# Optimization experiments

Hardware: AMD Instinct MI355X
Metric: run time of the kernel (lower is better)

## Reference

```python
import jax, jax.numpy as jnp
import numpy as np

N_NODES = 100000
N_EDGES = 3200000
ALPHA = 0.1
ITERATIONS = 10


def setup_inputs() -> dict:
    key = jax.random.key(0)
    ks = jax.random.split(key, 7)
    features = jax.random.normal(ks[0], (N_NODES, 512), dtype=jnp.float32)
    W1 = jax.random.normal(ks[1], (512, 64), dtype=jnp.float32) * 0.05
    b1 = jax.random.normal(ks[2], (64,), dtype=jnp.float32) * 0.05
    W2 = jax.random.normal(ks[3], (64, 64), dtype=jnp.float32) * 0.05
    b2 = jax.random.normal(ks[4], (64,), dtype=jnp.float32) * 0.05
    edge_weights = jax.random.uniform(ks[5], (N_EDGES,), dtype=jnp.float32)
    edge_index = jax.random.randint(ks[6], (2, N_EDGES), 0, N_NODES, dtype=jnp.int64)
    return {"features": features, "W1": W1, "b1": b1, "W2": W2, "b2": b2,
            "edge_weights": edge_weights, "edge_index": edge_index}


def reference(features, W1, b1, W2, b2, edge_weights, edge_index):
    # dense MLP head (dropout disabled / eval mode)
    h = jax.nn.relu(features @ W1 + b1)          # [N, hidden]
    z = h @ W2 + b2                              # [N, labels]

    row, col = edge_index[0], edge_index[1]

    def step(p, _):
        # SpMM: out[row] += w * p[col]
        gathered = edge_weights[:, None] * p[col]                 # [E, labels]
        new = jax.ops.segment_sum(gathered, row, num_segments=N_NODES)
        p = (1.0 - ALPHA) * new + ALPHA * z
        return p, None

    p, _ = jax.lax.scan(step, z, None, length=ITERATIONS)
    return p
```

## Files before the change

kernel.cpp:

```cpp
#include <hip/hip_runtime.h>
#include <hip/hip_fp16.h>
#include <cmath>

#define N_NODES 100000
#define N_EDGES 3200000
#define ALPHA   0.1f
#define ITERS   10
#define NBUK    1024
#define RPB     98
#define CHUNK   16384
#define NCH     196

typedef __attribute__((ext_vector_type(8))) short short8;
typedef __attribute__((ext_vector_type(4))) float f32x4;

__device__ __forceinline__ short f2bf(float x) {
    union { float f; unsigned u; } v; v.f = x;
    unsigned r = v.u + 0x7fffu + ((v.u >> 16) & 1u);
    return (short)(r >> 16);
}

__global__ void prep_w(const float* __restrict__ W1, const float* __restrict__ W2,
                       short* __restrict__ W1t, short* __restrict__ W2t)
{
    int t = blockIdx.x * 256 + threadIdx.x;
    if (t < 512 * 64) { int k = t >> 6, c = t & 63; W1t[c * 512 + k] = f2bf(W1[t]); }
    if (t < 64 * 64)  { int k = t >> 6, c = t & 63; W2t[c * 64 + k]  = f2bf(W2[t]); }
}

__global__ __launch_bounds__(256) void mlp_mfma(
    const float* __restrict__ F, const short* __restrict__ W1t,
    const short* __restrict__ W2t, const float* __restrict__ b1,
    const float* __restrict__ b2, __half* __restrict__ q0)
{
    __shared__ short Ft[64 * 128];
    __shared__ short Ht[64 * 64];

    const int t  = threadIdx.x;
    const int l  = t & 63;
    const int wv = t >> 6;
    const int wr = wv * 16;
    const long base = (long)blockIdx.x * 64;

    const int sr = t >> 4;
    const int sk = (t & 15) * 8;

    float4 f0a, f0b, f1a, f1b, f2a, f2b, f3a, f3b;

#define LOAD_TILE(kt) do {                                                   \
    long g0 = base + sr;      if (g0 > N_NODES - 1) g0 = N_NODES - 1;        \
    long g1 = base + sr + 16; if (g1 > N_NODES - 1) g1 = N_NODES - 1;        \
    long g2 = base + sr + 32; if (g2 > N_NODES - 1) g2 = N_NODES - 1;        \
    long g3 = base + sr + 48; if (g3 > N_NODES - 1) g3 = N_NODES - 1;        \
    f0a = *(const float4*)(F + g0 * 512 + (kt) * 128 + sk);                  \
    f0b = *(const float4*)(F + g0 * 512 + (kt) * 128 + sk + 4);              \
    f1a = *(const float4*)(F + g1 * 512 + (kt) * 128 + sk);                  \
    f1b = *(const float4*)(F + g1 * 512 + (kt) * 128 + sk + 4);              \
    f2a = *(const float4*)(F + g2 * 512 + (kt) * 128 + sk);                  \
    f2b = *(const float4*)(F + g2 * 512 + (kt) * 128 + sk + 4);              \
    f3a = *(const float4*)(F + g3 * 512 + (kt) * 128 + sk);                  \
    f3b = *(const float4*)(F + g3 * 512 + (kt) * 128 + sk + 4);              \
} while (0)

#define STORE_ROW(row, fa, fb) do {                                          \
    int r_ = (row);                                                          \
    short8 s_ = { f2bf((fa).x), f2bf((fa).y), f2bf((fa).z), f2bf((fa).w),    \
                  f2bf((fb).x), f2bf((fb).y), f2bf((fb).z), f2bf((fb).w) };  \
    *(short8*)&Ft[(r_ * 128 + sk) ^ ((r_ & 7) << 3)] = s_;                   \
} while (0)

    LOAD_TILE(0);

    f32x4 acc[4] = {};
    for (int kt = 0; kt < 4; ++kt) {
        STORE_ROW(sr,      f0a, f0b);
        STORE_ROW(sr + 16, f1a, f1b);
        STORE_ROW(sr + 32, f2a, f2b);
        STORE_ROW(sr + 48, f3a, f3b);
        __syncthreads();
        if (kt < 3) LOAD_TILE(kt + 1);
#pragma unroll
        for (int kc = 0; kc < 4; ++kc) {
            int kb = kc * 32 + (l >> 4) * 8;
            int ar = wr + (l & 15);
            short8 a = *(const short8*)&Ft[(ar * 128 + kb) ^ ((ar & 7) << 3)];
#pragma unroll
            for (int n = 0; n < 4; ++n) {
                int bc = n * 16 + (l & 15);
                short8 b = *(const short8*)(W1t + bc * 512 + kt * 128 + kb);
                acc[n] = __builtin_amdgcn_mfma_f32_16x16x32_bf16(a, b, acc[n], 0, 0, 0);
            }
        }
        __syncthreads();
    }

#pragma unroll
    for (int n = 0; n < 4; ++n) {
        int col = n * 16 + (l & 15);
        float bv = b1[col];
#pragma unroll
        for (int i = 0; i < 4; ++i) {
            int row = wr + (l >> 4) * 4 + i;
            float hv = fmaxf(acc[n][i] + bv, 0.0f);
            Ht[(row * 64 + col) ^ ((row & 7) << 3)] = f2bf(hv);
        }
    }
    f32x4 acc2[4] = {};
#pragma unroll
    for (int kc = 0; kc < 2; ++kc) {
        int kb = kc * 32 + (l >> 4) * 8;
        int ar = wr + (l & 15);
        short8 a = *(const short8*)&Ht[(ar * 64 + kb) ^ ((ar & 7) << 3)];
#pragma unroll
        for (int n = 0; n < 4; ++n) {
            int bc = n * 16 + (l & 15);
            short8 b = *(const short8*)(W2t + bc * 64 + kb);
            acc2[n] = __builtin_amdgcn_mfma_f32_16x16x32_bf16(a, b, acc2[n], 0, 0, 0);
        }
    }
#pragma unroll
    for (int n = 0; n < 4; ++n) {
        int col = n * 16 + (l & 15);
        float bv = b2[col];
#pragma unroll
        for (int i = 0; i < 4; ++i) {
            long row = base + wr + (l >> 4) * 4 + i;
            if (row < N_NODES)
                q0[row * 64 + col] = __float2half(acc2[n][i] + bv);
        }
    }
#undef LOAD_TILE
#undef STORE_ROW
}

__global__ __launch_bounds__(256) void bhist(const int* __restrict__ rows, int* __restrict__ gh)
{
    __shared__ int cnt[NBUK];
    for (int i = threadIdx.x; i < NBUK; i += 256) cnt[i] = 0;
    __syncthreads();
    int base = blockIdx.x * CHUNK;
    int end  = base + CHUNK; if (end > N_EDGES) end = N_EDGES;
    for (int i = base + threadIdx.x; i < end; i += 256)
        atomicAdd(&cnt[rows[i] / RPB], 1);
    __syncthreads();
    for (int i = threadIdx.x; i < NBUK; i += 256)
        gh[i * NCH + blockIdx.x] = cnt[i];
}

__global__ __launch_bounds__(512) void bscan(int* __restrict__ gh, int* __restrict__ btot)
{
    __shared__ int s[512];
    int k = blockIdx.x;
    int t = threadIdx.x;
    int v = (t < NCH) ? gh[k * NCH + t] : 0;
    s[t] = v;
    __syncthreads();
    for (int off = 1; off < 512; off <<= 1) {
        int x = (t >= off) ? s[t - off] : 0;
        __syncthreads();
        s[t] += x;
        __syncthreads();
    }
    if (t < NCH) gh[k * NCH + t] = s[t] - v;
    if (t == NCH - 1) btot[k] = s[t];
}

__global__ __launch_bounds__(1024) void scan_btot(const int* __restrict__ btot, int* __restrict__ bbase)
{
    __shared__ int s[1024];
    int t = threadIdx.x;
    int v = btot[t];
    s[t] = v;
    __syncthreads();
    for (int off = 1; off < 1024; off <<= 1) {
        int x = (t >= off) ? s[t - off] : 0;
        __syncthreads();
        s[t] += x;
        __syncthreads();
    }
    bbase[t] = s[t] - v;
}

__global__ __launch_bounds__(256) void bpart(const int* __restrict__ rows, const int* __restrict__ cols,
                                             const float* __restrict__ w, const int* __restrict__ gh,
                                             const int* __restrict__ bbase, uint2* __restrict__ stg)
{
    __shared__ int cur[NBUK];
    int blk = blockIdx.x;
    for (int i = threadIdx.x; i < NBUK; i += 256)
        cur[i] = bbase[i] + gh[i * NCH + blk];
    __syncthreads();
    int base = blk * CHUNK;
    int end  = base + CHUNK; if (end > N_EDGES) end = N_EDGES;
    for (int i = base + threadIdx.x; i < end; i += 256) {
        int r = rows[i];
        int b = r / RPB;
        int pos = atomicAdd(&cur[b], 1);
        float ws = w[i] * ((1.0f - ALPHA) / 16.0f);
        unsigned meta = (unsigned)cols[i] | ((unsigned)(r - b * RPB) << 17);
        stg[pos] = make_uint2(meta, __float_as_uint(ws));
    }
}

__global__ __launch_bounds__(256) void bucket_sort2(const int* __restrict__ bbase,
                                                    const uint2* __restrict__ stg,
                                                    unsigned long long* __restrict__ cw,
                                                    int* __restrict__ rowp)
{
    __shared__ int ldeg[RPB];
    __shared__ int lcur[RPB];
    __shared__ int sc[128];
    const int b = blockIdx.x;
    const int rowlo = b * RPB;
    if (rowlo >= N_NODES) return;
    int rowhi = rowlo + RPB; if (rowhi > N_NODES) rowhi = N_NODES;
    const int nrows = rowhi - rowlo;
    const int t = threadIdx.x;
    const int base = bbase[b];
    const int cnt = ((b + 1 < NBUK) ? bbase[b + 1] : N_EDGES) - base;

    if (t < RPB) ldeg[t] = 0;
    __syncthreads();
    for (int j = t; j < cnt; j += 256)
        atomicAdd(&ldeg[stg[base + j].x >> 17], 1);
    __syncthreads();
    int v = 0;
    if (t < 128) { v = (t < nrows) ? ldeg[t] : 0; sc[t] = v; }
    __syncthreads();
    for (int off = 1; off < 128; off <<= 1) {
        int x = (t < 128 && t >= off) ? sc[t - off] : 0;
        __syncthreads();
        if (t < 128) sc[t] += x;
        __syncthreads();
    }
    if (t < nrows) {
        int rp = base + sc[t] - v;
        rowp[rowlo + t] = rp;
        lcur[t] = rp;
    }
    if (t == 0 && rowhi == N_NODES) rowp[N_NODES] = base + cnt;
    __syncthreads();
    for (int j = t; j < cnt; j += 256) {
        uint2 rec = stg[base + j];
        int roff = rec.x >> 17;
        unsigned col = rec.x & 0x1FFFFu;
        int pos = atomicAdd(&lcur[roff], 1);
        cw[pos] = (unsigned long long)col | ((unsigned long long)rec.y << 32);
    }
}

template <int LAST>
__global__ __launch_bounds__(256) void spmm_kernel(
    const int* __restrict__ rowp, const unsigned long long* __restrict__ cw,
    const __half* __restrict__ qin, const __half* __restrict__ zh,
    float beta, float outscale,
    __half* __restrict__ qout, float* __restrict__ out)
{
    const int wid = blockIdx.x * 4 + (threadIdx.x >> 6);
    if (wid >= N_NODES) return;
    const int lane = threadIdx.x & 63;
    const int sub  = lane >> 3;
    const int l8   = lane & 7;

    const int start = rowp[wid];
    const int end   = rowp[wid + 1];

    uint4 zv = *(const uint4*)(zh + (long)wid * 64 + l8 * 8);

    float a0 = 0, a1 = 0, a2 = 0, a3 = 0, a4 = 0, a5 = 0, a6 = 0, a7 = 0;

#define ACC_EDGE(pc, v)                                                       \
    do {                                                                      \
        float ww_ = __uint_as_float((unsigned)((pc) >> 32));                  \
        float2 p_;                                                            \
        p_ = __half22float2(*(__half2*)&(v).x); a0 += ww_ * p_.x; a1 += ww_ * p_.y; \
        p_ = __half22float2(*(__half2*)&(v).y); a2 += ww_ * p_.x; a3 += ww_ * p_.y; \
        p_ = __half22float2(*(__half2*)&(v).z); a4 += ww_ * p_.x; a5 += ww_ * p_.y; \
        p_ = __half22float2(*(__half2*)&(v).w); a6 += ww_ * p_.x; a7 += ww_ * p_.y; \
    } while (0)

    int e = start + sub;
    for (; e + 24 < end; e += 32) {
        unsigned long long pc0 = cw[e];
        unsigned long long pc1 = cw[e + 8];
        unsigned long long pc2 = cw[e + 16];
        unsigned long long pc3 = cw[e + 24];
        uint4 v0 = *(const uint4*)(qin + (long)(unsigned)pc0 * 64 + l8 * 8);
        uint4 v1 = *(const uint4*)(qin + (long)(unsigned)pc1 * 64 + l8 * 8);
        uint4 v2 = *(const uint4*)(qin + (long)(unsigned)pc2 * 64 + l8 * 8);
        uint4 v3 = *(const uint4*)(qin + (long)(unsigned)pc3 * 64 + l8 * 8);
        ACC_EDGE(pc0, v0);
        ACC_EDGE(pc1, v1);
        ACC_EDGE(pc2, v2);
        ACC_EDGE(pc3, v3);
    }
    for (; e < end; e += 8) {
        unsigned long long pc = cw[e];
        uint4 v = *(const uint4*)(qin + (long)(unsigned)pc * 64 + l8 * 8);
        ACC_EDGE(pc, v);
    }
#undef ACC_EDGE

    a0 += __shfl_xor(a0, 8);  a1 += __shfl_xor(a1, 8);
    a2 += __shfl_xor(a2, 8);  a3 += __shfl_xor(a3, 8);
    a4 += __shfl_xor(a4, 8);  a5 += __shfl_xor(a5, 8);
    a6 += __shfl_xor(a6, 8);  a7 += __shfl_xor(a7, 8);
    a0 += __shfl_xor(a0, 16); a1 += __shfl_xor(a1, 16);
    a2 += __shfl_xor(a2, 16); a3 += __shfl_xor(a3, 16);
    a4 += __shfl_xor(a4, 16); a5 += __shfl_xor(a5, 16);
    a6 += __shfl_xor(a6, 16); a7 += __shfl_xor(a7, 16);
    a0 += __shfl_xor(a0, 32); a1 += __shfl_xor(a1, 32);
    a2 += __shfl_xor(a2, 32); a3 += __shfl_xor(a3, 32);
    a4 += __shfl_xor(a4, 32); a5 += __shfl_xor(a5, 32);
    a6 += __shfl_xor(a6, 32); a7 += __shfl_xor(a7, 32);

    if (lane < 8) {
        float2 z0 = __half22float2(*(__half2*)&zv.x);
        float2 z1 = __half22float2(*(__half2*)&zv.y);
        float2 z2 = __half22float2(*(__half2*)&zv.z);
        float2 z3 = __half22float2(*(__half2*)&zv.w);
        float o0 = a0 + beta * z0.x, o1 = a1 + beta * z0.y;
        float o2 = a2 + beta * z1.x, o3 = a3 + beta * z1.y;
        float o4 = a4 + beta * z2.x, o5 = a5 + beta * z2.y;
        float o6 = a6 + beta * z3.x, o7 = a7 + beta * z3.y;
        if (LAST) {
            float4 ra = { outscale * o0, outscale * o1, outscale * o2, outscale * o3 };
            float4 rb = { outscale * o4, outscale * o5, outscale * o6, outscale * o7 };
            *(float4*)(out + (long)wid * 64 + lane * 8)     = ra;
            *(float4*)(out + (long)wid * 64 + lane * 8 + 4) = rb;
        } else {
            __half2 h0 = __floats2half2_rn(o0, o1);
            __half2 h1 = __floats2half2_rn(o2, o3);
            __half2 h2 = __floats2half2_rn(o4, o5);
            __half2 h3 = __floats2half2_rn(o6, o7);
            uint4 pv = { *(unsigned*)&h0, *(unsigned*)&h1, *(unsigned*)&h2, *(unsigned*)&h3 };
            *(uint4*)(qout + (long)wid * 64 + lane * 8) = pv;
        }
    }
}

extern "C" void kernel_launch(void* const* d_in, const int* in_sizes, int n_in,
                              void* d_out, int out_size, void* d_ws, size_t ws_size,
                              hipStream_t stream)
{
    const float* features = (const float*)d_in[0];
    const float* W1 = (const float*)d_in[1];
    const float* b1 = (const float*)d_in[2];
    const float* W2 = (const float*)d_in[3];
    const float* b2 = (const float*)d_in[4];
    const float* ew = (const float*)d_in[5];
    const int*   ei = (const int*)d_in[6];
    const int* erow = ei;
    const int* ecol = ei + N_EDGES;
    float* out = (float*)d_out;

    char* ws = (char*)d_ws;
    size_t off = 0;
    auto alloc = [&](size_t bytes) {
        size_t c = off;
        off += (bytes + 255) & ~(size_t)255;
        return c;
    };
    __half* q0    = (__half*)(ws + alloc((size_t)N_NODES * 64 * 2));
    __half* qA    = (__half*)(ws + alloc((size_t)N_NODES * 64 * 2));
    __half* qB    = (__half*)(ws + alloc((size_t)N_NODES * 64 * 2));
    unsigned long long* cw = (unsigned long long*)(ws + alloc((size_t)N_EDGES * 8));
    uint2* stg    = (uint2*)(ws + alloc((size_t)N_EDGES * 8));
    int*   gh     = (int*)  (ws + alloc((size_t)NBUK * NCH * 4));
    short* W1t    = (short*)(ws + alloc((size_t)512 * 64 * 2));
    short* W2t    = (short*)(ws + alloc((size_t)64 * 64 * 2));
    int*   rowp   = (int*)  (ws + alloc((size_t)(N_NODES + 1) * 4));
    int*   btot   = (int*)  (ws + alloc((size_t)NBUK * 4));
    int*   bbase  = (int*)  (ws + alloc((size_t)NBUK * 4));
    (void)ws_size; (void)in_sizes; (void)n_in; (void)out_size;

    prep_w<<<128, 256, 0, stream>>>(W1, W2, W1t, W2t);
    mlp_mfma<<<(N_NODES + 63) / 64, 256, 0, stream>>>(features, W1t, W2t, b1, b2, q0);

    bhist<<<NCH, 256, 0, stream>>>(erow, gh);
    bscan<<<NBUK, 512, 0, stream>>>(gh, btot);
    scan_btot<<<1, 1024, 0, stream>>>(btot, bbase);
    bpart<<<NCH, 256, 0, stream>>>(erow, ecol, ew, gh, bbase, stg);
    bucket_sort2<<<NBUK, 256, 0, stream>>>(bbase, stg, cw, rowp);

    const __half* qi = q0;
    for (int it = 1; it < ITERS; ++it) {
        __half* qo = (it & 1) ? qA : qB;
        float beta = (float)(0.1 / pow(16.0, (double)it));
        spmm_kernel<0><<<(N_NODES + 3) / 4, 256, 0, stream>>>(rowp, cw, qi, q0, beta, 1.0f, qo, nullptr);
        qi = qo;
    }
    float beta10 = (float)(0.1 / pow(16.0, 10.0));
    float osc    = (float)pow(16.0, 10.0);
    spmm_kernel<1><<<(N_NODES + 3) / 4, 256, 0, stream>>>(rowp, cw, qi, q0, beta10, osc, nullptr, out);
}
```

Baseline: 802.8 us.

## Shrink MLP tile to 32 rows, halve histogram chunk, reduce SpMM unroll

```diff
diff --git a/kernel.cpp b/kernel.cpp
--- a/kernel.cpp
+++ b/kernel.cpp
@@ -8,8 +8,8 @@
 #define ITERS   10
 #define NBUK    1024
 #define RPB     98
-#define CHUNK   16384
-#define NCH     196
+#define CHUNK   8192
+#define NCH     391
 
 typedef __attribute__((ext_vector_type(8))) short short8;
 typedef __attribute__((ext_vector_type(4))) float f32x4;
@@ -28,55 +28,48 @@
     if (t < 64 * 64)  { int k = t >> 6, c = t & 63; W2t[c * 64 + k]  = f2bf(W2[t]); }
 }
 
-__global__ __launch_bounds__(256) void mlp_mfma(
+__global__ __launch_bounds__(128) void mlp_mfma(
     const float* __restrict__ F, const short* __restrict__ W1t,
     const short* __restrict__ W2t, const float* __restrict__ b1,
     const float* __restrict__ b2, __half* __restrict__ q0)
 {
-    __shared__ short Ft[64 * 128];
-    __shared__ short Ht[64 * 64];
+    __shared__ short Ft[32 * 128];
+    __shared__ short Ht[32 * 64];
 
     const int t  = threadIdx.x;
     const int l  = t & 63;
     const int wv = t >> 6;
     const int wr = wv * 16;
-    const long base = (long)blockIdx.x * 64;
-
-    const int sr = t >> 4;
-    const int sk = (t & 15) * 8;
-
-    float4 f0a, f0b, f1a, f1b, f2a, f2b, f3a, f3b;
+    const long base = (long)blockIdx.x * 32;
+
+    const int sr = t >> 2;
+    const int ck = (t & 3) * 32;
+
+    float4 f0, f1, f2, f3, f4, f5, f6, f7;
 
 #define LOAD_TILE(kt) do {                                                   \
-    long g0 = base + sr;      if (g0 > N_NODES - 1) g0 = N_NODES - 1;        \
-    long g1 = base + sr + 16; if (g1 > N_NODES - 1) g1 = N_NODES - 1;        \
-    long g2 = base + sr + 32; if (g2 > N_NODES - 1) g2 = N_NODES - 1;        \
-    long g3 = base + sr + 48; if (g3 > N_NODES - 1) g3 = N_NODES - 1;        \
-    f0a = *(const float4*)(F + g0 * 512 + (kt) * 128 + sk);                  \
-    f0b = *(const float4*)(F + g0 * 512 + (kt) * 128 + sk + 4);              \
-    f1a = *(const float4*)(F + g1 * 512 + (kt) * 128 + sk);                  \
-    f1b = *(const float4*)(F + g1 * 512 + (kt) * 128 + sk + 4);              \
-    f2a = *(const float4*)(F + g2 * 512 + (kt) * 128 + sk);                  \
-    f2b = *(const float4*)(F + g2 * 512 + (kt) * 128 + sk + 4);              \
-    f3a = *(const float4*)(F + g3 * 512 + (kt) * 128 + sk);                  \
-    f3b = *(const float4*)(F + g3 * 512 + (kt) * 128 + sk + 4);              \
+    const float* p_ = F + (base + sr) * 512 + (kt) * 128 + ck;               \
+    f0 = *(const float4*)(p_ +  0);  f1 = *(const float4*)(p_ +  4);         \
+    f2 = *(const float4*)(p_ +  8);  f3 = *(const float4*)(p_ + 12);         \
+    f4 = *(const float4*)(p_ + 16);  f5 = *(const float4*)(p_ + 20);         \
+    f6 = *(const float4*)(p_ + 24);  f7 = *(const float4*)(p_ + 28);         \
 } while (0)
 
-#define STORE_ROW(row, fa, fb) do {                                          \
-    int r_ = (row);                                                          \
+#define STORE_PAIR(j2, fa, fb) do {                                          \
+    int k_ = ck + (j2) * 8;                                                  \
     short8 s_ = { f2bf((fa).x), f2bf((fa).y), f2bf((fa).z), f2bf((fa).w),    \
                   f2bf((fb).x), f2bf((fb).y), f2bf((fb).z), f2bf((fb).w) };  \
-    *(short8*)&Ft[(r_ * 128 + sk) ^ ((r_ & 7) << 3)] = s_;                   \
+    *(short8*)&Ft[(sr * 128 + k_) ^ ((sr & 7) << 3)] = s_;                   \
 } while (0)
 
     LOAD_TILE(0);
 
     f32x4 acc[4] = {};
     for (int kt = 0; kt < 4; ++kt) {
-        STORE_ROW(sr,      f0a, f0b);
-        STORE_ROW(sr + 16, f1a, f1b);
-        STORE_ROW(sr + 32, f2a, f2b);
-        STORE_ROW(sr + 48, f3a, f3b);
+        STORE_PAIR(0, f0, f1);
+        STORE_PAIR(1, f2, f3);
+        STORE_PAIR(2, f4, f5);
+        STORE_PAIR(3, f6, f7);
         __syncthreads();
         if (kt < 3) LOAD_TILE(kt + 1);
 #pragma unroll
@@ -125,12 +118,11 @@
 #pragma unroll
         for (int i = 0; i < 4; ++i) {
             long row = base + wr + (l >> 4) * 4 + i;
-            if (row < N_NODES)
-                q0[row * 64 + col] = __float2half(acc2[n][i] + bv);
+            q0[row * 64 + col] = __float2half(acc2[n][i] + bv);
         }
     }
 #undef LOAD_TILE
-#undef STORE_ROW
+#undef STORE_PAIR
 }
 
 __global__ __launch_bounds__(256) void bhist(const int* __restrict__ rows, int* __restrict__ gh)
@@ -280,21 +272,15 @@
     } while (0)
 
     int e = start + sub;
-    for (; e + 24 < end; e += 32) {
+    for (; e + 8 < end; e += 16) {
         unsigned long long pc0 = cw[e];
         unsigned long long pc1 = cw[e + 8];
-        unsigned long long pc2 = cw[e + 16];
-        unsigned long long pc3 = cw[e + 24];
         uint4 v0 = *(const uint4*)(qin + (long)(unsigned)pc0 * 64 + l8 * 8);
         uint4 v1 = *(const uint4*)(qin + (long)(unsigned)pc1 * 64 + l8 * 8);
-        uint4 v2 = *(const uint4*)(qin + (long)(unsigned)pc2 * 64 + l8 * 8);
-        uint4 v3 = *(const uint4*)(qin + (long)(unsigned)pc3 * 64 + l8 * 8);
         ACC_EDGE(pc0, v0);
         ACC_EDGE(pc1, v1);
-        ACC_EDGE(pc2, v2);
-        ACC_EDGE(pc3, v3);
-    }
-    for (; e < end; e += 8) {
+    }
+    if (e < end) {
         unsigned long long pc = cw[e];
         uint4 v = *(const uint4*)(qin + (long)(unsigned)pc * 64 + l8 * 8);
         ACC_EDGE(pc, v);
@@ -375,7 +361,7 @@
     (void)ws_size; (void)in_sizes; (void)n_in; (void)out_size;
 
     prep_w<<<128, 256, 0, stream>>>(W1, W2, W1t, W2t);
-    mlp_mfma<<<(N_NODES + 63) / 64, 256, 0, stream>>>(features, W1t, W2t, b1, b2, q0);
+    mlp_mfma<<<N_NODES / 32, 128, 0, stream>>>(features, W1t, W2t, b1, b2, q0);
 
     bhist<<<NCH, 256, 0, stream>>>(erow, gh);
     bscan<<<NBUK, 512, 0, stream>>>(gh, btot);
```

After: 772.3 us. -3.8%, faster.
